# Kernel optimization log

Measured on AMD Instinct MI355X. Metric: run time of the kernel, lower is better.

## Reference

```python
import jax, jax.numpy as jnp
import numpy as np

N = 50000   # nodes
E = 600000  # edges
D = 128     # in = hidden = out channels
G = 256     # graphs in batch
EPS = 1e-5


def setup_inputs() -> dict:
    key = jax.random.key(0)
    ks = jax.random.split(key, 16)
    sc = 1.0 / np.sqrt(D)
    inp = {
        "x": jax.random.normal(ks[0], (N, D), jnp.float32),
        "edge_index": jax.random.randint(ks[1], (2, E), 0, N, dtype=jnp.int32),
        "edge_attr": jax.random.normal(ks[2], (E, 4), jnp.float32),
        "batch": jnp.sort(jax.random.randint(ks[3], (N,), 0, G, dtype=jnp.int32)),
        # conv1 + norm1
        "W1": jax.random.normal(ks[4], (D, D), jnp.float32) * sc,
        "b1": jnp.zeros((D,), jnp.float32),
        "g1": jnp.ones((D,), jnp.float32),
        "be1": jnp.zeros((D,), jnp.float32),
        # middle conv (num_layers=3 -> one hidden conv) + norm
        "Wm": jax.random.normal(ks[5], (D, D), jnp.float32) * sc,
        "bm": jnp.zeros((D,), jnp.float32),
        "gm": jnp.ones((D,), jnp.float32),
        "bem": jnp.zeros((D,), jnp.float32),
        # conv2 + norm2
        "W2": jax.random.normal(ks[6], (D, D), jnp.float32) * sc,
        "b2": jnp.zeros((D,), jnp.float32),
        "g2": jnp.ones((D,), jnp.float32),
        "be2": jnp.zeros((D,), jnp.float32),
    }
    return inp


def _gcn_conv(x, W, b, src, dst, dinv):
    # PyG GCNConv with add_self_loops=True: out = D^{-1/2}(A+I)D^{-1/2} (x W) + b
    h = x @ W
    enorm = dinv[src] * dinv[dst]                      # [E]
    msg = h[src] * enorm[:, None]                      # gather + scale
    agg = jnp.zeros_like(h).at[dst].add(msg)           # scatter-add to targets
    agg = agg + h * (dinv * dinv)[:, None]             # self-loop contribution
    return agg + b


def _bn(x, g, b):
    # BatchNorm1d over nodes (batch statistics)
    mu = jnp.mean(x, axis=0)
    var = jnp.var(x, axis=0)
    return (x - mu) * jax.lax.rsqrt(var + EPS) * g + b


def reference(x, edge_index, edge_attr, batch,
              W1, b1, g1, be1, Wm, bm, gm, bem, W2, b2, g2, be2):
    src, dst = edge_index[0], edge_index[1]
    # degree of A + I (in-degree at targets, +1 self loop); shared by all layers
    deg = jnp.zeros((N,), x.dtype).at[dst].add(1.0) + 1.0
    dinv = jax.lax.rsqrt(deg)

    h = jax.nn.relu(_bn(_gcn_conv(x, W1, b1, src, dst, dinv), g1, be1))
    h = jax.nn.relu(_bn(_gcn_conv(h, Wm, bm, src, dst, dinv), gm, bem))
    h = _bn(_gcn_conv(h, W2, b2, src, dst, dinv), g2, be2)

    # global mean pool (batch re-based at batch[0])
    seg = batch - batch[0]
    sums = jax.ops.segment_sum(h, seg, num_segments=G)
    cnt = jax.ops.segment_sum(jnp.ones((N,), h.dtype), seg, num_segments=G)
    return sums / jnp.maximum(cnt, 1.0)[:, None]
```

## Files before the change

### kernel.cpp

```cpp
#include <hip/hip_runtime.h>

#define DIM 128
constexpr float EPS = 1e-5f;
#define NSHARD 32
#define SHARD (NSHARD * 256)

typedef _Float16 f16;
typedef __attribute__((ext_vector_type(8))) _Float16 f16x8;
typedef __attribute__((ext_vector_type(4))) float f32x4;

__global__ __launch_bounds__(256) void k_prep(const int* __restrict__ dst,
                                              int* __restrict__ degi, int E,
                                              const float* __restrict__ W0,
                                              const float* __restrict__ W1,
                                              const float* __restrict__ W2,
                                              f16* __restrict__ wt) {
    if (blockIdx.x < 12) {
        int layer = blockIdx.x >> 2;
        int quarter = blockIdx.x & 3;
        const float* W = layer == 0 ? W0 : (layer == 1 ? W1 : W2);
        f16* hi = wt + (size_t)layer * DIM * DIM;
        for (int idx = quarter * 4096 + threadIdx.x; idx < (quarter + 1) * 4096;
             idx += 256) {
            int k = idx >> 7, c = idx & 127;
            hi[c * DIM + k] = (f16)W[idx];
        }
    } else {
        int e = (blockIdx.x - 12) * 256 + threadIdx.x;
        if (e < E) atomicAdd(&degi[dst[e]], 1);
    }
}

__global__ __launch_bounds__(256) void k_scan_local(const int* __restrict__ degi,
                                                    int* __restrict__ row_ptr,
                                                    float* __restrict__ dinv,
                                                    int* __restrict__ bsum, int n) {
    __shared__ int ws[4];
    int t = threadIdx.x, lane = t & 63, wv = t >> 6;
    int i0 = blockIdx.x * 1024 + t * 4;
    int v[4];
#pragma unroll
    for (int j = 0; j < 4; ++j) {
        int i = i0 + j;
        v[j] = (i < n) ? degi[i] : 0;
        if (i < n) dinv[i] = rsqrtf((float)v[j] + 1.0f);
    }
    int tsum = v[0] + v[1] + v[2] + v[3];
    int sc = tsum;
#pragma unroll
    for (int off = 1; off < 64; off <<= 1) {
        int u = __shfl_up(sc, off, 64);
        if (lane >= off) sc += u;
    }
    if (lane == 63) ws[wv] = sc;
    __syncthreads();
    int woff = 0;
    for (int j = 0; j < wv; ++j) woff += ws[j];
    int run = woff + sc - tsum;
#pragma unroll
    for (int j = 0; j < 4; ++j) {
        int i = i0 + j;
        if (i < n) row_ptr[i] = run;
        run += v[j];
    }
    if (t == 255) bsum[blockIdx.x] = woff + sc;
}

__global__ __launch_bounds__(256) void k_scan_add(int* __restrict__ row_ptr,
                                                  int* __restrict__ cursor,
                                                  const int* __restrict__ bsum,
                                                  int n, int E, int nb) {
    __shared__ int soff;
    int t = threadIdx.x;
    int seg = blockIdx.x >> 2;
    if (t < 64) {
        int v = (t < nb) ? bsum[t] : 0;
        int sc = v;
#pragma unroll
        for (int off = 1; off < 64; off <<= 1) {
            int u = __shfl_up(sc, off, 64);
            if (t >= off) sc += u;
        }
        if (t == seg) soff = sc - v;
    }
    __syncthreads();
    int i = blockIdx.x * 256 + t;
    if (i < n) {
        int v = row_ptr[i] + soff;
        row_ptr[i] = v;
        cursor[i] = v;
    }
    if (i == 0) row_ptr[n] = E;
}

__global__ void k_fill(const int* __restrict__ src, const int* __restrict__ dst,
                       int* __restrict__ cursor, int* __restrict__ csr_src, int E) {
    int e = blockIdx.x * blockDim.x + threadIdx.x;
    if (e >= E) return;
    int d = dst[e];
    int slot = atomicAdd(&cursor[d], 1);
    csr_src[slot] = src[e];
}

template <bool PRE_BN>
__global__ __launch_bounds__(256) void k_matmul_mfma(
    const float* __restrict__ inF, const f16* __restrict__ inH,
    const f16* __restrict__ wt, const float* __restrict__ dinv,
    const float* __restrict__ stats, const float* __restrict__ g,
    const float* __restrict__ be, float inv_n, f16* __restrict__ out, int n) {
    __shared__ __align__(16) char sA[64 * 256];
    __shared__ float sScale[DIM], sShift[DIM];

    int t = threadIdx.x;
    int w = t >> 6, l = t & 63;

    if (PRE_BN) {
        if (t < DIM) {
            float su = 0.f, sq = 0.f;
            for (int s = 0; s < NSHARD; ++s) {
                su += stats[s * 256 + t];
                sq += stats[s * 256 + 128 + t];
            }
            float mu = su * inv_n;
            float var = sq * inv_n - mu * mu;
            float sc = rsqrtf(var + EPS) * g[t];
            sScale[t] = sc;
            sShift[t] = be[t] - mu * sc;
        }
        __syncthreads();
    }

    f16x8 bh[2][4];
    {
        int col = w * 32 + (l & 15);
        int ksub = (l >> 4) * 8;
#pragma unroll
        for (int ct = 0; ct < 2; ++ct) {
            int c2 = col + ct * 16;
#pragma unroll
            for (int kt = 0; kt < 4; ++kt)
                bh[ct][kt] = *(const f16x8*)&wt[(size_t)c2 * DIM + kt * 32 + ksub];
        }
    }

#pragma unroll
    for (int half = 0; half < 2; ++half) {
        int row0 = blockIdx.x * 128 + half * 64;
        if (row0 >= n) break;
        if (half == 1) __syncthreads();

        {
            int r = t >> 2;
            int row_g = row0 + r;
            if (row_g >= n) row_g = n - 1;
            int cbase = (t & 3) * 32;
#pragma unroll
            for (int o = 0; o < 4; ++o) {
                int c0 = cbase + o * 8;
                f16x8 h8;
                if (PRE_BN) {
                    f16x8 v8 = *(const f16x8*)(inH + (size_t)row_g * DIM + c0);
#pragma unroll
                    for (int j = 0; j < 8; ++j) {
                        float v = (float)v8[j] * sScale[c0 + j] + sShift[c0 + j];
                        h8[j] = (f16)fmaxf(v, 0.f);
                    }
                } else {
                    float4 v0 = *(const float4*)(inF + (size_t)row_g * DIM + c0);
                    float4 v1 = *(const float4*)(inF + (size_t)row_g * DIM + c0 + 4);
                    h8[0] = (f16)v0.x; h8[1] = (f16)v0.y; h8[2] = (f16)v0.z; h8[3] = (f16)v0.w;
                    h8[4] = (f16)v1.x; h8[5] = (f16)v1.y; h8[6] = (f16)v1.z; h8[7] = (f16)v1.w;
                }
                int byte = (r * 256 + c0 * 2) ^ ((r & 7) << 4);
                *(f16x8*)(sA + byte) = h8;
            }
        }
        __syncthreads();

        f32x4 acc[4][2];
#pragma unroll
        for (int rt = 0; rt < 4; ++rt)
#pragma unroll
            for (int ct = 0; ct < 2; ++ct) acc[rt][ct] = (f32x4){0.f, 0.f, 0.f, 0.f};

#pragma unroll
        for (int rt = 0; rt < 4; ++rt) {
            int row_l = rt * 16 + (l & 15);
            int kb = (l >> 4) * 16;
            f16x8 a[4];
#pragma unroll
            for (int kt = 0; kt < 4; ++kt) {
                int byte = (row_l * 256 + kt * 64 + kb) ^ ((row_l & 7) << 4);
                a[kt] = *(const f16x8*)(sA + byte);
            }
#pragma unroll
            for (int ct = 0; ct < 2; ++ct) {
                f32x4 c = acc[rt][ct];
#pragma unroll
                for (int kt = 0; kt < 4; ++kt)
                    c = __builtin_amdgcn_mfma_f32_16x16x32_f16(a[kt], bh[ct][kt], c, 0, 0, 0);
                acc[rt][ct] = c;
            }
        }

        int colw = w * 32 + (l & 15);
#pragma unroll
        for (int rt = 0; rt < 4; ++rt) {
            int row_l = rt * 16 + ((l >> 4) << 2);
#pragma unroll
            for (int reg = 0; reg < 4; ++reg) {
                int gr = row0 + row_l + reg;
                if (gr >= n) continue;
                float dv = dinv[gr];
#pragma unroll
                for (int ct = 0; ct < 2; ++ct)
                    out[(size_t)gr * DIM + colw + ct * 16] = (f16)(acc[rt][ct][reg] * dv);
            }
        }
    }
}

template <bool POOL>
__global__ __launch_bounds__(256) void k_gs(const f16* __restrict__ hs,
                                            const int* __restrict__ csr_src,
                                            const int* __restrict__ row_ptr,
                                            const float* __restrict__ dinv,
                                            const float* __restrict__ b,
                                            const int* __restrict__ batch,
                                            f16* __restrict__ agg,
                                            float* __restrict__ stats_part,
                                            float* __restrict__ gsum, int n) {
    __shared__ float sSum[4][DIM];
    __shared__ float sSq[4][DIM];
    __shared__ int sSeg[4];

    int t = threadIdx.x;
    int wv = t >> 6, l = t & 63;
    int node = blockIdx.x * 4 + wv;
    int grp = l >> 4;
    int c8 = (l & 15) * 8;
    bool valid = node < n;

    f16x8 hv = {};
    if (valid && grp == 0) hv = *(const f16x8*)(hs + (size_t)node * DIM + c8);

    float acc[8] = {};
    int beg = 0, end = 0;
    if (valid) {
        beg = row_ptr[node];
        end = row_ptr[node + 1];
    }
    for (int e = beg + grp; e < end; e += 16) {
        bool v1 = e + 4 < end, v2 = e + 8 < end, v3 = e + 12 < end;
        f16x8 a0 = *(const f16x8*)(hs + (size_t)csr_src[e] * DIM + c8);
        f16x8 a1 = {}, a2 = {}, a3 = {};
        if (v1) a1 = *(const f16x8*)(hs + (size_t)csr_src[e + 4] * DIM + c8);
        if (v2) a2 = *(const f16x8*)(hs + (size_t)csr_src[e + 8] * DIM + c8);
        if (v3) a3 = *(const f16x8*)(hs + (size_t)csr_src[e + 12] * DIM + c8);
#pragma unroll
        for (int j = 0; j < 8; ++j)
            acc[j] += ((float)a0[j] + (float)a1[j]) + ((float)a2[j] + (float)a3[j]);
    }
#pragma unroll
    for (int j = 0; j < 8; ++j) {
        acc[j] += __shfl_xor(acc[j], 16, 64);
        acc[j] += __shfl_xor(acc[j], 32, 64);
    }

    if (grp == 0) {
        if (valid) {
            float dv = dinv[node];
            f32x4 bb0 = *(const f32x4*)(b + c8);
            f32x4 bb1 = *(const f32x4*)(b + c8 + 4);
            float o[8];
#pragma unroll
            for (int j = 0; j < 4; ++j) {
                o[j] = (acc[j] + (float)hv[j]) * dv + bb0[j];
                o[j + 4] = (acc[j + 4] + (float)hv[j + 4]) * dv + bb1[j];
            }
            f16x8 ov;
#pragma unroll
            for (int j = 0; j < 8; ++j) ov[j] = (f16)o[j];
            *(f16x8*)(agg + (size_t)node * DIM + c8) = ov;
            f32x4 s0 = {o[0], o[1], o[2], o[3]}, s1 = {o[4], o[5], o[6], o[7]};
            f32x4 q0 = {o[0]*o[0], o[1]*o[1], o[2]*o[2], o[3]*o[3]};
            f32x4 q1 = {o[4]*o[4], o[5]*o[5], o[6]*o[6], o[7]*o[7]};
            *(f32x4*)&sSum[wv][c8] = s0;
            *(f32x4*)&sSum[wv][c8 + 4] = s1;
            *(f32x4*)&sSq[wv][c8] = q0;
            *(f32x4*)&sSq[wv][c8 + 4] = q1;
            if (POOL && l == 0) sSeg[wv] = batch[node] - batch[0];
        } else {
            f32x4 z = {0.f, 0.f, 0.f, 0.f};
            *(f32x4*)&sSum[wv][c8] = z;
            *(f32x4*)&sSum[wv][c8 + 4] = z;
            *(f32x4*)&sSq[wv][c8] = z;
            *(f32x4*)&sSq[wv][c8 + 4] = z;
            if (POOL && l == 0) sSeg[wv] = -1;
        }
    }
    __syncthreads();

    int shard = (blockIdx.x & (NSHARD - 1)) * 256;
    if (t < 128) {
        float s = sSum[0][t] + sSum[1][t] + sSum[2][t] + sSum[3][t];
        atomicAdd(&stats_part[shard + t], s);
    } else {
        int ch = t - 128;
        float s = sSq[0][ch] + sSq[1][ch] + sSq[2][ch] + sSq[3][ch];
        atomicAdd(&stats_part[shard + 128 + ch], s);
    }

    if (POOL && t < 128) {
        int cur = -1;
        float a = 0.f;
#pragma unroll
        for (int w = 0; w < 4; ++w) {
            int sg = sSeg[w];
            if (sg < 0) continue;
            if (sg != cur) {
                if (cur >= 0) atomicAdd(&gsum[(size_t)cur * DIM + t], a);
                a = 0.f;
                cur = sg;
            }
            a += sSum[w][t];
        }
        if (cur >= 0) atomicAdd(&gsum[(size_t)cur * DIM + t], a);
    }
}

__global__ __launch_bounds__(128) void k_pool_fin(const float* __restrict__ gsum,
                                                  const int* __restrict__ batch,
                                                  const float* __restrict__ stats,
                                                  const float* __restrict__ g,
                                                  const float* __restrict__ be,
                                                  float* __restrict__ out,
                                                  int n, float inv_n) {
    int gseg = blockIdx.x;
    int c = threadIdx.x;
    int b0 = batch[0];
    int target = b0 + gseg;
    int lo = 0, hi = n;
    while (lo < hi) { int mid = (lo + hi) >> 1; if (batch[mid] < target) lo = mid + 1; else hi = mid; }
    int start = lo;
    lo = start; hi = n;
    while (lo < hi) { int mid = (lo + hi) >> 1; if (batch[mid] < target + 1) lo = mid + 1; else hi = mid; }
    int end = lo;
    int cnt = end - start;

    float su = 0.f, sq = 0.f;
    for (int s = 0; s < NSHARD; ++s) {
        su += stats[s * 256 + c];
        sq += stats[s * 256 + 128 + c];
    }
    float mu = su * inv_n;
    float var = sq * inv_n - mu * mu;
    float scale = rsqrtf(var + EPS) * g[c];
    float shift = be[c] - mu * scale;
    float o = 0.f;
    if (cnt > 0) o = (gsum[(size_t)gseg * DIM + c] / (float)cnt) * scale + shift;
    out[(size_t)gseg * DIM + c] = o;
}

extern "C" void kernel_launch(void* const* d_in, const int* in_sizes, int n_in,
                              void* d_out, int out_size, void* d_ws, size_t ws_size,
                              hipStream_t stream) {
    const float* x = (const float*)d_in[0];
    const int* edge_index = (const int*)d_in[1];
    const int* batch = (const int*)d_in[3];
    const float* W1 = (const float*)d_in[4];
    const float* b1 = (const float*)d_in[5];
    const float* g1 = (const float*)d_in[6];
    const float* be1 = (const float*)d_in[7];
    const float* Wm = (const float*)d_in[8];
    const float* bm = (const float*)d_in[9];
    const float* gm = (const float*)d_in[10];
    const float* bem = (const float*)d_in[11];
    const float* W2 = (const float*)d_in[12];
    const float* b2 = (const float*)d_in[13];
    const float* g2 = (const float*)d_in[14];
    const float* be2 = (const float*)d_in[15];

    int n = in_sizes[0] / DIM;
    int E = in_sizes[1] / 2;
    int G = out_size / DIM;

    const int* srcI = edge_index;
    const int* dstI = edge_index + E;

    char* p = (char*)d_ws;
    f16* bufA = (f16*)p;                p += (size_t)n * DIM * 2;
    f16* bufB = (f16*)p;                p += (size_t)n * DIM * 2;
    float* dinv = (float*)p;            p += (size_t)n * 4;
    int* row_ptr = (int*)p;             p += (size_t)(n + 1) * 4;
    int* cursor = (int*)p;              p += (size_t)n * 4;
    int* csr_src = (int*)p;             p += (size_t)E * 4;
    int* bsum = (int*)p;                p += 64 * 4;
    char* zero0 = p;
    int* degi = (int*)p;                p += (size_t)n * 4;
    float* stats3 = (float*)p;          p += 3 * SHARD * 4;
    float* gsum = (float*)p;            p += (size_t)G * DIM * 4;
    size_t zero_bytes = (size_t)(p - zero0);
    f16* wsplit = (f16*)p;              p += (size_t)3 * DIM * DIM * 2;

    float* out = (float*)d_out;
    float inv_n = 1.0f / (float)n;
    int nb = (n + 1023) / 1024;

    hipMemsetAsync(zero0, 0, zero_bytes, stream);
    k_prep<<<12 + (E + 255) / 256, 256, 0, stream>>>(dstI, degi, E, W1, Wm, W2, wsplit);
    k_scan_local<<<nb, 256, 0, stream>>>(degi, row_ptr, dinv, bsum, n);
    k_scan_add<<<(n + 255) / 256, 256, 0, stream>>>(row_ptr, cursor, bsum, n, E, nb);
    k_fill<<<(E + 255) / 256, 256, 0, stream>>>(srcI, dstI, cursor, csr_src, E);

    struct Layer { const float *b, *g, *be; };
    Layer L[3] = {{b1, g1, be1}, {bm, gm, bem}, {b2, g2, be2}};

    int mmBlocks = (n + 127) / 128;
    int gsBlocks = (n + 3) / 4;
    for (int l = 0; l < 3; ++l) {
        const f16* wl = wsplit + (size_t)l * DIM * DIM;
        float* stats_l = stats3 + l * SHARD;
        if (l == 0)
            k_matmul_mfma<false><<<mmBlocks, 256, 0, stream>>>(
                x, nullptr, wl, dinv, nullptr, nullptr, nullptr, inv_n, bufA, n);
        else
            k_matmul_mfma<true><<<mmBlocks, 256, 0, stream>>>(
                nullptr, bufB, wl, dinv, stats3 + (l - 1) * SHARD,
                L[l - 1].g, L[l - 1].be, inv_n, bufA, n);
        if (l < 2)
            k_gs<false><<<gsBlocks, 256, 0, stream>>>(bufA, csr_src, row_ptr, dinv,
                                                      L[l].b, batch, bufB, stats_l,
                                                      nullptr, n);
        else
            k_gs<true><<<gsBlocks, 256, 0, stream>>>(bufA, csr_src, row_ptr, dinv,
                                                     L[l].b, batch, bufB, stats_l,
                                                     gsum, n);
    }

    k_pool_fin<<<G, 128, 0, stream>>>(gsum, batch, stats3 + 2 * SHARD, g2, be2,
                                      out, n, inv_n);
}
```

Measured before the change: 251.0 us.

## Merge CSR fill into first matmul launch and sum gathered rows in fp16

The CSR fill kernel is folded into the layer-0 matmul launch as extra blocks, so the atomic scatter of edge sources runs alongside the MFMA work in one dispatch and a separate kernel launch goes away. The gather loop now adds the four gathered fp16 vectors in fp16 before converting once to fp32, which cuts conversion and add instructions. The fp16 partial sums lose some precision compared with accumulating every term in fp32.

```diff
diff --git a/kernel.cpp b/kernel.cpp
--- a/kernel.cpp
+++ b/kernel.cpp
@@ -93,21 +93,13 @@
     if (i == 0) row_ptr[n] = E;
 }
 
-__global__ void k_fill(const int* __restrict__ src, const int* __restrict__ dst,
-                       int* __restrict__ cursor, int* __restrict__ csr_src, int E) {
-    int e = blockIdx.x * blockDim.x + threadIdx.x;
-    if (e >= E) return;
-    int d = dst[e];
-    int slot = atomicAdd(&cursor[d], 1);
-    csr_src[slot] = src[e];
-}
-
 template <bool PRE_BN>
-__global__ __launch_bounds__(256) void k_matmul_mfma(
+__device__ __forceinline__ void mm_body(
     const float* __restrict__ inF, const f16* __restrict__ inH,
     const f16* __restrict__ wt, const float* __restrict__ dinv,
     const float* __restrict__ stats, const float* __restrict__ g,
-    const float* __restrict__ be, float inv_n, f16* __restrict__ out, int n) {
+    const float* __restrict__ be, float inv_n, f16* __restrict__ out,
+    int n, int bid) {
     __shared__ __align__(16) char sA[64 * 256];
     __shared__ float sScale[DIM], sShift[DIM];
 
@@ -145,7 +137,7 @@
 
 #pragma unroll
     for (int half = 0; half < 2; ++half) {
-        int row0 = blockIdx.x * 128 + half * 64;
+        int row0 = bid * 128 + half * 64;
         if (row0 >= n) break;
         if (half == 1) __syncthreads();
 
@@ -218,6 +210,33 @@
             }
         }
     }
+}
+
+template <bool PRE_BN>
+__global__ __launch_bounds__(256) void k_matmul_mfma(
+    const float* __restrict__ inF, const f16* __restrict__ inH,
+    const f16* __restrict__ wt, const float* __restrict__ dinv,
+    const float* __restrict__ stats, const float* __restrict__ g,
+    const float* __restrict__ be, float inv_n, f16* __restrict__ out, int n) {
+    mm_body<PRE_BN>(inF, inH, wt, dinv, stats, g, be, inv_n, out, n, blockIdx.x);
+}
+
+__global__ __launch_bounds__(256) void k_mm0_fill(
+    const float* __restrict__ inF, const f16* __restrict__ wt,
+    const float* __restrict__ dinv, f16* __restrict__ out, int n, int mmBlocks,
+    const int* __restrict__ src, const int* __restrict__ dst,
+    int* __restrict__ cursor, int* __restrict__ csr_src, int E) {
+    if ((int)blockIdx.x >= mmBlocks) {
+        int e = ((int)blockIdx.x - mmBlocks) * 256 + threadIdx.x;
+        if (e < E) {
+            int d = dst[e];
+            int slot = atomicAdd(&cursor[d], 1);
+            csr_src[slot] = src[e];
+        }
+        return;
+    }
+    mm_body<false>(inF, nullptr, wt, dinv, nullptr, nullptr, nullptr, 1.0f, out, n,
+                   blockIdx.x);
 }
 
 template <bool POOL>
@@ -257,9 +276,9 @@
         if (v1) a1 = *(const f16x8*)(hs + (size_t)csr_src[e + 4] * DIM + c8);
         if (v2) a2 = *(const f16x8*)(hs + (size_t)csr_src[e + 8] * DIM + c8);
         if (v3) a3 = *(const f16x8*)(hs + (size_t)csr_src[e + 12] * DIM + c8);
-#pragma unroll
-        for (int j = 0; j < 8; ++j)
-            acc[j] += ((float)a0[j] + (float)a1[j]) + ((float)a2[j] + (float)a3[j]);
+        f16x8 s = (a0 + a1) + (a2 + a3);
+#pragma unroll
+        for (int j = 0; j < 8; ++j) acc[j] += (float)s[j];
     }
 #pragma unroll
     for (int j = 0; j < 8; ++j) {
@@ -411,23 +430,26 @@
     k_prep<<<12 + (E + 255) / 256, 256, 0, stream>>>(dstI, degi, E, W1, Wm, W2, wsplit);
     k_scan_local<<<nb, 256, 0, stream>>>(degi, row_ptr, dinv, bsum, n);
     k_scan_add<<<(n + 255) / 256, 256, 0, stream>>>(row_ptr, cursor, bsum, n, E, nb);
-    k_fill<<<(E + 255) / 256, 256, 0, stream>>>(srcI, dstI, cursor, csr_src, E);
 
     struct Layer { const float *b, *g, *be; };
     Layer L[3] = {{b1, g1, be1}, {bm, gm, bem}, {b2, g2, be2}};
 
     int mmBlocks = (n + 127) / 128;
+    int fillBlocks = (E + 255) / 256;
     int gsBlocks = (n + 3) / 4;
-    for (int l = 0; l < 3; ++l) {
+
+    k_mm0_fill<<<mmBlocks + fillBlocks, 256, 0, stream>>>(
+        x, wsplit, dinv, bufA, n, mmBlocks, srcI, dstI, cursor, csr_src, E);
+    k_gs<false><<<gsBlocks, 256, 0, stream>>>(bufA, csr_src, row_ptr, dinv,
+                                              L[0].b, batch, bufB, stats3,
+                                              nullptr, n);
+
+    for (int l = 1; l < 3; ++l) {
         const f16* wl = wsplit + (size_t)l * DIM * DIM;
         float* stats_l = stats3 + l * SHARD;
-        if (l == 0)
-            k_matmul_mfma<false><<<mmBlocks, 256, 0, stream>>>(
-                x, nullptr, wl, dinv, nullptr, nullptr, nullptr, inv_n, bufA, n);
-        else
-            k_matmul_mfma<true><<<mmBlocks, 256, 0, stream>>>(
-                nullptr, bufB, wl, dinv, stats3 + (l - 1) * SHARD,
-                L[l - 1].g, L[l - 1].be, inv_n, bufA, n);
+        k_matmul_mfma<true><<<mmBlocks, 256, 0, stream>>>(
+            nullptr, bufB, wl, dinv, stats3 + (l - 1) * SHARD,
+            L[l - 1].g, L[l - 1].be, inv_n, bufA, n);
         if (l < 2)
             k_gs<false><<<gsBlocks, 256, 0, stream>>>(bufA, csr_src, row_ptr, dinv,
                                                       L[l].b, batch, bufB, stats_l,
```

Measured after the change: 238.9 us. -4.8%, faster.
